# Kernel tuning notes

Hardware: AMD Instinct MI355X
Metric: run time of the kernel (lower is better)

Reference implementation:

```python
import jax, jax.numpy as jnp
import numpy as np
import math

FEATURE_DIMS = 6
D_HIDDEN = 32
N_TOKENS = 2097152
NUM_SEGMENTS = 8192
SCALE = 400.0 / math.log(10.0)


def setup_inputs() -> dict:
    key = jax.random.key(0)
    ks = jax.random.split(key, 8)
    x = jax.random.normal(ks[0], (N_TOKENS, FEATURE_DIMS), dtype=jnp.float32)
    segment_ids = jnp.sort(jax.random.randint(ks[1], (N_TOKENS,), 0, NUM_SEGMENTS)).astype(jnp.int32)
    # params (kaiming-ish init, same layout as nn.Linear: y = x @ W.T + b -> stored pre-transposed)
    W1 = jax.random.normal(ks[2], (FEATURE_DIMS, D_HIDDEN), dtype=jnp.float32) / np.sqrt(FEATURE_DIMS)
    b1 = jax.random.normal(ks[3], (D_HIDDEN,), dtype=jnp.float32) * 0.01
    wr = jax.random.normal(ks[4], (D_HIDDEN,), dtype=jnp.float32) / np.sqrt(D_HIDDEN)
    br = jax.random.normal(ks[5], (), dtype=jnp.float32) * 0.01
    wz = jax.random.normal(ks[6], (D_HIDDEN,), dtype=jnp.float32) / np.sqrt(D_HIDDEN)
    bz = jax.random.normal(ks[7], (), dtype=jnp.float32) * 0.01
    return {"x": x, "W1": W1, "b1": b1, "wr": wr, "br": br, "wz": wz, "bz": bz,
            "segment_ids": segment_ids, "num_segments": NUM_SEGMENTS}


def reference(x, W1, b1, wr, br, wz, bz, segment_ids, num_segments):
    # layer1: Linear + ReLU  -> h [N, d_hidden]
    h = jax.nn.relu(x @ W1 + b1)
    # rating / weight heads, squeezed to [N]
    r = h @ wr + br
    z = h @ wz + bz
    # per-segment (per-game) softmax over z, weighted sum of r -- single pass, no Python loop
    zmax = jax.ops.segment_max(z, segment_ids, num_segments=num_segments)  # [G], -inf for empty
    e = jnp.exp(z - zmax[segment_ids])                                      # [N]
    num = jax.ops.segment_sum(e * r, segment_ids, num_segments=num_segments)  # [G]
    den = jax.ops.segment_sum(e, segment_ids, num_segments=num_segments)      # [G]
    den_safe = jnp.where(den > 0, den, 1.0)
    preds = jnp.where(den > 0, num / den_safe, 0.0)  # empty segment -> 0, as in the torch code
    return SCALE * preds
```

## Files before the change

### kernel.cpp

```cpp
#include <hip/hip_runtime.h>
#include <hip/hip_bf16.h>

#define SCALE_F 173.71779276130078f
#define TPT 8
#define BLOCK 256

__global__ void zero_ws_kernel(float* ws, int n) {
    int i = blockIdx.x * 256 + threadIdx.x;
    if (i < n) ws[i] = 0.0f;
}

__global__ __launch_bounds__(BLOCK) void strength_main_kernel(
    const float* __restrict__ x,
    const float* __restrict__ W1,
    const float* __restrict__ b1,
    const float* __restrict__ wr,
    const float* __restrict__ brp,
    const float* __restrict__ wz,
    const float* __restrict__ bzp,
    const int*   __restrict__ seg_ids,
    long N,
    float* __restrict__ num,
    float* __restrict__ den)
{
    __shared__ float Wl[192];
    __shared__ float b1l[32], wrl[32], wzl[32];

    const int tid  = threadIdx.x;
    const int lane = tid & 63;

    if (tid < 192) Wl[tid] = W1[tid];
    if (tid < 32) { b1l[tid] = b1[tid]; wrl[tid] = wr[tid]; wzl[tid] = wz[tid]; }
    __syncthreads();

    const float brv = *brp;
    const float bzv = *bzp;

    const long base = (long)blockIdx.x * (BLOCK * TPT) + (long)(tid >> 6) * (64 * TPT) + lane;

    float xv[TPT][6];
    int   sg[TPT];

    #pragma unroll
    for (int k = 0; k < TPT; ++k) {
        long t = base + (long)k * 64;
        if (t < N) {
            const float* xp = x + t * 6;
            float2 a = *reinterpret_cast<const float2*>(xp + 0);
            float2 b = *reinterpret_cast<const float2*>(xp + 2);
            float2 c = *reinterpret_cast<const float2*>(xp + 4);
            xv[k][0] = a.x; xv[k][1] = a.y;
            xv[k][2] = b.x; xv[k][3] = b.y;
            xv[k][4] = c.x; xv[k][5] = c.y;
            sg[k] = seg_ids[t];
        } else {
            #pragma unroll
            for (int i = 0; i < 6; ++i) xv[k][i] = 0.0f;
            sg[k] = 0x7fffffff;
        }
    }

    float r[TPT], z[TPT];
    #pragma unroll
    for (int k = 0; k < TPT; ++k) { r[k] = brv; z[k] = bzv; }

    #pragma unroll 4
    for (int j = 0; j < 32; ++j) {
        const float w0 = Wl[0 * 32 + j];
        const float w1 = Wl[1 * 32 + j];
        const float w2 = Wl[2 * 32 + j];
        const float w3 = Wl[3 * 32 + j];
        const float w4 = Wl[4 * 32 + j];
        const float w5 = Wl[5 * 32 + j];
        const float bj  = b1l[j];
        const float wrj = wrl[j];
        const float wzj = wzl[j];
        #pragma unroll
        for (int k = 0; k < TPT; ++k) {
            float h = fmaf(xv[k][0], w0,
                      fmaf(xv[k][1], w1,
                      fmaf(xv[k][2], w2,
                      fmaf(xv[k][3], w3,
                      fmaf(xv[k][4], w4,
                      fmaf(xv[k][5], w5, bj))))));
            h = fmaxf(h, 0.0f);
            r[k] = fmaf(h, wrj, r[k]);
            z[k] = fmaf(h, wzj, z[k]);
        }
    }

    #pragma unroll
    for (int k = 0; k < TPT; ++k) {
        long t = base + (long)k * 64;
        bool valid = (t < N);
        int   s  = sg[k];
        float e  = valid ? __expf(z[k]) : 0.0f;
        float er = e * r[k];

        #pragma unroll
        for (int d = 1; d < 64; d <<= 1) {
            float e2  = __shfl_up(e, d);
            float er2 = __shfl_up(er, d);
            int   s2  = __shfl_up(s, d);
            if (lane >= d && s2 == s) { e += e2; er += er2; }
        }
        int snext = __shfl_down(s, 1);
        bool last = (lane == 63) || (snext != s);
        if (last && valid) {
            atomicAdd(&den[s], e);
            atomicAdd(&num[s], er);
        }
    }
}

__global__ void finalize_kernel(const float* __restrict__ num,
                                const float* __restrict__ den,
                                float* __restrict__ out, int G) {
    int g = blockIdx.x * 256 + threadIdx.x;
    if (g < G) {
        float d = den[g];
        out[g] = (d > 0.0f) ? (SCALE_F * num[g] / d) : 0.0f;
    }
}

extern "C" void kernel_launch(void* const* d_in, const int* in_sizes, int n_in,
                              void* d_out, int out_size, void* d_ws, size_t ws_size,
                              hipStream_t stream) {
    const float* x   = (const float*)d_in[0];
    const float* W1  = (const float*)d_in[1];
    const float* b1  = (const float*)d_in[2];
    const float* wr  = (const float*)d_in[3];
    const float* br  = (const float*)d_in[4];
    const float* wz  = (const float*)d_in[5];
    const float* bz  = (const float*)d_in[6];
    const int*   seg = (const int*)d_in[7];

    long N = in_sizes[7];
    int  G = out_size;

    float* num = (float*)d_ws;
    float* den = num + G;
    float* out = (float*)d_out;

    int zn = 2 * G;
    zero_ws_kernel<<<(zn + 255) / 256, 256, 0, stream>>>(num, zn);

    long tokens_per_block = (long)BLOCK * TPT;
    int  nblocks = (int)((N + tokens_per_block - 1) / tokens_per_block);
    strength_main_kernel<<<nblocks, BLOCK, 0, stream>>>(
        x, W1, b1, wr, br, wz, bz, seg, N, num, den);

    finalize_kernel<<<(G + 255) / 256, 256, 0, stream>>>(num, den, out, G);
}
```

Before: 34.56 us.

## Use contiguous per-thread tokens with shared-memory segment bins instead of wave scans

```diff
diff --git a/kernel.cpp b/kernel.cpp
--- a/kernel.cpp
+++ b/kernel.cpp
@@ -1,11 +1,11 @@
 #include <hip/hip_runtime.h>
-#include <hip/hip_bf16.h>
 
 #define SCALE_F 173.71779276130078f
+#define BLOCK 256
 #define TPT 8
-#define BLOCK 256
+#define NBINS 64
 
-__global__ void zero_ws_kernel(float* ws, int n) {
+__global__ void zero_ws_kernel(float* __restrict__ ws, int n) {
     int i = blockIdx.x * 256 + threadIdx.x;
     if (i < n) ws[i] = 0.0f;
 }
@@ -18,97 +18,124 @@
     const float* __restrict__ brp,
     const float* __restrict__ wz,
     const float* __restrict__ bzp,
-    const int*   __restrict__ seg_ids,
-    long N,
+    const int*   __restrict__ seg,
+    int N, int G,
     float* __restrict__ num,
     float* __restrict__ den)
 {
-    __shared__ float Wl[192];
-    __shared__ float b1l[32], wrl[32], wzl[32];
+    __shared__ float4 WB[6][8];
+    __shared__ float4 B1s[8], WRs[8], WZs[8];
+    __shared__ float  binE[NBINS], binR[NBINS];
+    __shared__ int    baseSeg_s;
 
-    const int tid  = threadIdx.x;
-    const int lane = tid & 63;
+    const int tid = threadIdx.x;
 
-    if (tid < 192) Wl[tid] = W1[tid];
-    if (tid < 32) { b1l[tid] = b1[tid]; wrl[tid] = wr[tid]; wzl[tid] = wz[tid]; }
+    if (tid < 48)                 ((float4*)WB)[tid]  = ((const float4*)W1)[tid];
+    else if (tid < 56)            B1s[tid - 48]       = ((const float4*)b1)[tid - 48];
+    else if (tid < 64)            WRs[tid - 56]       = ((const float4*)wr)[tid - 56];
+    else if (tid < 72)            WZs[tid - 64]       = ((const float4*)wz)[tid - 64];
+    if (tid < NBINS) { binE[tid] = 0.0f; binR[tid] = 0.0f; }
+    if (tid == 0) {
+        long t = (long)blockIdx.x * (BLOCK * TPT);
+        baseSeg_s = seg[t < N ? t : (N - 1)];
+    }
     __syncthreads();
+    const int baseSeg = baseSeg_s;
+
+    const long t0   = (long)blockIdx.x * (BLOCK * TPT) + (long)tid * TPT;
+    const int  kmax = (t0 >= N) ? 0 : (int)((N - t0 < TPT) ? (N - t0) : TPT);
+
+    float a[TPT * 6];
+    int   sg[TPT];
+    if (kmax == TPT) {
+        const float4* xp = (const float4*)(x + (size_t)t0 * 6);
+        #pragma unroll
+        for (int i = 0; i < 12; ++i) {
+            float4 v = xp[i];
+            a[4 * i + 0] = v.x; a[4 * i + 1] = v.y;
+            a[4 * i + 2] = v.z; a[4 * i + 3] = v.w;
+        }
+        const int4* sp = (const int4*)(seg + t0);
+        int4 s0 = sp[0], s1 = sp[1];
+        sg[0] = s0.x; sg[1] = s0.y; sg[2] = s0.z; sg[3] = s0.w;
+        sg[4] = s1.x; sg[5] = s1.y; sg[6] = s1.z; sg[7] = s1.w;
+    } else {
+        #pragma unroll
+        for (int k = 0; k < TPT; ++k) {
+            if (k < kmax) {
+                const float* xp = x + (size_t)(t0 + k) * 6;
+                #pragma unroll
+                for (int i = 0; i < 6; ++i) a[k * 6 + i] = xp[i];
+                sg[k] = seg[t0 + k];
+            } else {
+                #pragma unroll
+                for (int i = 0; i < 6; ++i) a[k * 6 + i] = 0.0f;
+                sg[k] = -1;
+            }
+        }
+    }
 
     const float brv = *brp;
     const float bzv = *bzp;
-
-    const long base = (long)blockIdx.x * (BLOCK * TPT) + (long)(tid >> 6) * (64 * TPT) + lane;
-
-    float xv[TPT][6];
-    int   sg[TPT];
-
-    #pragma unroll
-    for (int k = 0; k < TPT; ++k) {
-        long t = base + (long)k * 64;
-        if (t < N) {
-            const float* xp = x + t * 6;
-            float2 a = *reinterpret_cast<const float2*>(xp + 0);
-            float2 b = *reinterpret_cast<const float2*>(xp + 2);
-            float2 c = *reinterpret_cast<const float2*>(xp + 4);
-            xv[k][0] = a.x; xv[k][1] = a.y;
-            xv[k][2] = b.x; xv[k][3] = b.y;
-            xv[k][4] = c.x; xv[k][5] = c.y;
-            sg[k] = seg_ids[t];
-        } else {
-            #pragma unroll
-            for (int i = 0; i < 6; ++i) xv[k][i] = 0.0f;
-            sg[k] = 0x7fffffff;
-        }
-    }
 
     float r[TPT], z[TPT];
     #pragma unroll
     for (int k = 0; k < TPT; ++k) { r[k] = brv; z[k] = bzv; }
 
-    #pragma unroll 4
-    for (int j = 0; j < 32; ++j) {
-        const float w0 = Wl[0 * 32 + j];
-        const float w1 = Wl[1 * 32 + j];
-        const float w2 = Wl[2 * 32 + j];
-        const float w3 = Wl[3 * 32 + j];
-        const float w4 = Wl[4 * 32 + j];
-        const float w5 = Wl[5 * 32 + j];
-        const float bj  = b1l[j];
-        const float wrj = wrl[j];
-        const float wzj = wzl[j];
+    #pragma unroll
+    for (int jb = 0; jb < 8; ++jb) {
+        const float4 w0 = WB[0][jb], w1 = WB[1][jb], w2 = WB[2][jb];
+        const float4 w3 = WB[3][jb], w4 = WB[4][jb], w5 = WB[5][jb];
+        const float4 bb = B1s[jb], rr = WRs[jb], zz = WZs[jb];
         #pragma unroll
         for (int k = 0; k < TPT; ++k) {
-            float h = fmaf(xv[k][0], w0,
-                      fmaf(xv[k][1], w1,
-                      fmaf(xv[k][2], w2,
-                      fmaf(xv[k][3], w3,
-                      fmaf(xv[k][4], w4,
-                      fmaf(xv[k][5], w5, bj))))));
-            h = fmaxf(h, 0.0f);
-            r[k] = fmaf(h, wrj, r[k]);
-            z[k] = fmaf(h, wzj, z[k]);
+            const float* xk = &a[k * 6];
+            {   float h = fmaf(xk[0], w0.x, fmaf(xk[1], w1.x, fmaf(xk[2], w2.x,
+                          fmaf(xk[3], w3.x, fmaf(xk[4], w4.x, fmaf(xk[5], w5.x, bb.x))))));
+                h = fmaxf(h, 0.0f); r[k] = fmaf(h, rr.x, r[k]); z[k] = fmaf(h, zz.x, z[k]); }
+            {   float h = fmaf(xk[0], w0.y, fmaf(xk[1], w1.y, fmaf(xk[2], w2.y,
+                          fmaf(xk[3], w3.y, fmaf(xk[4], w4.y, fmaf(xk[5], w5.y, bb.y))))));
+                h = fmaxf(h, 0.0f); r[k] = fmaf(h, rr.y, r[k]); z[k] = fmaf(h, zz.y, z[k]); }
+            {   float h = fmaf(xk[0], w0.z, fmaf(xk[1], w1.z, fmaf(xk[2], w2.z,
+                          fmaf(xk[3], w3.z, fmaf(xk[4], w4.z, fmaf(xk[5], w5.z, bb.z))))));
+                h = fmaxf(h, 0.0f); r[k] = fmaf(h, rr.z, r[k]); z[k] = fmaf(h, zz.z, z[k]); }
+            {   float h = fmaf(xk[0], w0.w, fmaf(xk[1], w1.w, fmaf(xk[2], w2.w,
+                          fmaf(xk[3], w3.w, fmaf(xk[4], w4.w, fmaf(xk[5], w5.w, bb.w))))));
+                h = fmaxf(h, 0.0f); r[k] = fmaf(h, rr.w, r[k]); z[k] = fmaf(h, zz.w, z[k]); }
         }
     }
 
-    #pragma unroll
-    for (int k = 0; k < TPT; ++k) {
-        long t = base + (long)k * 64;
-        bool valid = (t < N);
-        int   s  = sg[k];
-        float e  = valid ? __expf(z[k]) : 0.0f;
-        float er = e * r[k];
+    {
+        int   cur = (kmax > 0) ? sg[0] : -1;
+        float ce = 0.0f, cer = 0.0f;
+        #pragma unroll
+        for (int k = 0; k < TPT; ++k) {
+            if (k < kmax) {
+                float e  = __expf(z[k]);
+                float er = e * r[k];
+                if (sg[k] != cur) {
+                    int b = cur - baseSeg;
+                    if ((unsigned)b < NBINS) { atomicAdd(&binE[b], ce); atomicAdd(&binR[b], cer); }
+                    else                     { atomicAdd(&den[cur], ce); atomicAdd(&num[cur], cer); }
+                    cur = sg[k]; ce = 0.0f; cer = 0.0f;
+                }
+                ce += e; cer += er;
+            }
+        }
+        if (kmax > 0) {
+            int b = cur - baseSeg;
+            if ((unsigned)b < NBINS) { atomicAdd(&binE[b], ce); atomicAdd(&binR[b], cer); }
+            else                     { atomicAdd(&den[cur], ce); atomicAdd(&num[cur], cer); }
+        }
+    }
 
-        #pragma unroll
-        for (int d = 1; d < 64; d <<= 1) {
-            float e2  = __shfl_up(e, d);
-            float er2 = __shfl_up(er, d);
-            int   s2  = __shfl_up(s, d);
-            if (lane >= d && s2 == s) { e += e2; er += er2; }
-        }
-        int snext = __shfl_down(s, 1);
-        bool last = (lane == 63) || (snext != s);
-        if (last && valid) {
+    __syncthreads();
+    if (tid < NBINS) {
+        float e = binE[tid];
+        if (e != 0.0f) {
+            int s = baseSeg + tid;
             atomicAdd(&den[s], e);
-            atomicAdd(&num[s], er);
+            atomicAdd(&num[s], binR[tid]);
         }
     }
 }
@@ -135,8 +162,8 @@
     const float* bz  = (const float*)d_in[6];
     const int*   seg = (const int*)d_in[7];
 
-    long N = in_sizes[7];
-    int  G = out_size;
+    int N = in_sizes[7];
+    int G = out_size;
 
     float* num = (float*)d_ws;
     float* den = num + G;
@@ -146,9 +173,9 @@
     zero_ws_kernel<<<(zn + 255) / 256, 256, 0, stream>>>(num, zn);
 
     long tokens_per_block = (long)BLOCK * TPT;
-    int  nblocks = (int)((N + tokens_per_block - 1) / tokens_per_block);
+    int  nblocks = (int)(((long)N + tokens_per_block - 1) / tokens_per_block);
     strength_main_kernel<<<nblocks, BLOCK, 0, stream>>>(
-        x, W1, b1, wr, br, wz, bz, seg, N, num, den);
+        x, W1, b1, wr, br, wz, bz, seg, N, G, num, den);
 
     finalize_kernel<<<(G + 255) / 256, 256, 0, stream>>>(num, den, out, G);
 }
```

After: 55.12 us. 59.5% more time.
